# Kernel optimization log

Hardware: AMD Instinct MI355X
Metric: run time of the kernel (lower is better)

The kernel has to match this reference:

```python
import jax, jax.numpy as jnp
import numpy as np

HDIM = 256
VOCAB = 100000
NUM_CLASSES = 5
N_LEAVES = 2048


def _build_tree(n_leaves):
    # balanced pairing tree; leaves are nodes [0, n_leaves), internal nodes appended
    # in topological order so every parent index > its children's indices.
    frontier = list(range(n_leaves)); nid = n_leaves; left = []; right = []
    while len(frontier) > 1:
        nxt = []
        for a, b in zip(frontier[0::2], frontier[1::2]):
            left.append(a); right.append(b); nxt.append(nid); nid += 1
        if len(frontier) % 2 == 1:
            nxt.append(frontier[-1])
        frontier = nxt
    return np.asarray(left, np.int64), np.asarray(right, np.int64)


def setup_inputs() -> dict:
    key = jax.random.key(0)
    ks = jax.random.split(key, 12)
    left, right = _build_tree(N_LEAVES)
    s = 1.0 / float(np.sqrt(HDIM))
    W = lambda k, shp: (jax.random.normal(k, shp, jnp.float32) * s)
    z = lambda n: jnp.zeros((n,), jnp.float32)
    return {
        "word_ids": jax.random.randint(ks[0], (N_LEAVES,), 0, VOCAB),
        "left_idx": jnp.asarray(left),
        "right_idx": jnp.asarray(right),
        "emb": jax.random.normal(ks[1], (VOCAB, HDIM), jnp.float32) * 0.1,
        "Wi": W(ks[2], (HDIM, HDIM)), "bi": z(HDIM),
        "Wo": W(ks[3], (HDIM, HDIM)), "bo": z(HDIM),
        "Wu": W(ks[4], (HDIM, HDIM)), "bu": z(HDIM),
        "Ui": W(ks[5], (HDIM, 2 * HDIM)), "bui": z(HDIM),
        "Uo": W(ks[6], (HDIM, 2 * HDIM)), "buo": z(HDIM),
        "Uu": W(ks[7], (HDIM, 2 * HDIM)), "buu": z(HDIM),
        "Uf1": W(ks[8], (HDIM, HDIM)), "bf1": z(HDIM),
        "Uf2": W(ks[9], (HDIM, HDIM)), "bf2": z(HDIM),
        "Wp": W(ks[10], (NUM_CLASSES, HDIM)), "bp": z(NUM_CLASSES),
    }


def reference(word_ids, left_idx, right_idx, emb,
              Wi, bi, Wo, bo, Wu, bu,
              Ui, bui, Uo, buo, Uu, buu,
              Uf1, bf1, Uf2, bf2, Wp, bp):
    sig = jax.nn.sigmoid
    relu = jax.nn.relu
    n_leaves = word_ids.shape[0]
    n_internal = left_idx.shape[0]
    n_nodes = n_leaves + n_internal

    # --- leaf nodes, fully vectorized ---
    e = emb[word_ids]                                  # [L, H]
    i = sig(e @ Wi.T + bi)
    o = sig(e @ Wo.T + bo)
    u = relu(e @ Wu.T + bu)
    c_leaf = i * u
    h_leaf = o * relu(c_leaf)

    h_buf = jnp.zeros((n_nodes, HDIM), e.dtype).at[:n_leaves].set(h_leaf)
    node_ids = jnp.arange(n_leaves, n_nodes)

    # --- internal nodes: sequential by topological order ---
    def step(hb, xs):
        l, r, idx = xs
        lh = hb[l]; rh = hb[r]                         # [H] each
        cat = jnp.concatenate([lh, rh])                # [2H]
        ii = sig(Ui @ cat + bui)
        oo = sig(Uo @ cat + buo)
        uu = relu(Uu @ cat + buu)
        # NOTE: faithful to source — forget gates multiply child h, not child c
        c = ii * uu + sig(Uf1 @ lh + bf1) * lh + sig(Uf2 @ rh + bf2) * rh
        h = oo * relu(c)
        return hb.at[idx].set(h), None

    h_buf, _ = jax.lax.scan(step, h_buf, (left_idx, right_idx, node_ids))

    # per-node class logits (original concatenates projection(h) across all nodes)
    logits = h_buf @ Wp.T + bp                         # [n_nodes, numClasses]
    return logits
```

## Files before the change

kernel.cpp:

```cpp
#include <hip/hip_runtime.h>
#include <math.h>

#define H 256
#define KT 32
#define KTILES 16

__device__ __forceinline__ float sigmoidf_(float x) {
    return 1.0f / (1.0f + expf(-x));
}

__global__ __launch_bounds__(256) void pack_weights_kernel(
    const float* __restrict__ Wi, const float* __restrict__ Wo, const float* __restrict__ Wu,
    const float* __restrict__ Ui, const float* __restrict__ Uo, const float* __restrict__ Uu,
    const float* __restrict__ Uf1, const float* __restrict__ Uf2,
    float* __restrict__ dst)
{
    long idx = (long)blockIdx.x * 256 + threadIdx.x;
    const long W4N = 4L * 512 * 256;
    if (idx < W4N) {
        long g = idx >> 17;
        long r = idx & 131071;
        long k = r >> 8;
        long j = r & 255;
        float v;
        if      (g == 0) v = Ui[j * 512 + k];
        else if (g == 1) v = Uo[j * 512 + k];
        else if (g == 2) v = Uu[j * 512 + k];
        else             v = (k < 256) ? Uf1[j * 256 + k] : Uf2[j * 256 + (k - 256)];
        dst[idx] = v;
    } else {
        long t = idx - W4N;
        long g = t >> 16;
        long r = t & 65535;
        long k = r >> 8;
        long j = r & 255;
        const float* src = (g == 0) ? Wi : (g == 1) ? Wo : Wu;
        dst[idx] = src[j * 256 + k];
    }
}

template<int LPB>
__global__ __launch_bounds__(256) void leaf_kernel(
    const int* __restrict__ word_ids, const float* __restrict__ emb,
    const float* __restrict__ W3,
    const float* __restrict__ bi, const float* __restrict__ bo, const float* __restrict__ bu,
    float* __restrict__ h_buf)
{
    const int j = threadIdx.x;
    const int lbase = blockIdx.x * LPB;
    int wid[LPB];
#pragma unroll
    for (int l = 0; l < LPB; ++l)
        wid[l] = __builtin_amdgcn_readfirstlane(word_ids[lbase + l]);

    float ai[LPB], ao[LPB], au[LPB];
#pragma unroll
    for (int l = 0; l < LPB; ++l) { ai[l] = 0.f; ao[l] = 0.f; au[l] = 0.f; }

    const float* WiT = W3;
    const float* WoT = W3 + 65536;
    const float* WuT = W3 + 131072;

#pragma unroll 4
    for (int k = 0; k < H; ++k) {
        float wi = WiT[k * H + j];
        float wo = WoT[k * H + j];
        float wu = WuT[k * H + j];
#pragma unroll
        for (int l = 0; l < LPB; ++l) {
            float e = emb[(long)wid[l] * H + k];
            ai[l] = fmaf(e, wi, ai[l]);
            ao[l] = fmaf(e, wo, ao[l]);
            au[l] = fmaf(e, wu, au[l]);
        }
    }
    float bij = bi[j], boj = bo[j], buj = bu[j];
#pragma unroll
    for (int l = 0; l < LPB; ++l) {
        float ii = sigmoidf_(ai[l] + bij);
        float oo = sigmoidf_(ao[l] + boj);
        float uu = fmaxf(au[l] + buj, 0.f);
        float c  = ii * uu;
        float h  = oo * fmaxf(c, 0.f);
        h_buf[(long)(lbase + l) * H + j] = h;
    }
}

template<int NCH>
__global__ __launch_bounds__(256) void level_partial_kernel(
    const int* __restrict__ left_idx, const int* __restrict__ right_idx,
    const float* __restrict__ W4, const float* __restrict__ h_buf,
    float* __restrict__ part,
    int level_start, int chunk_base, int chunk_nodes, int n_leaves)
{
    const int j  = threadIdx.x;
    const int kt = blockIdx.x;
    const int nb = blockIdx.y * NCH;

    float w[4][KT];
#pragma unroll
    for (int g = 0; g < 4; ++g)
#pragma unroll
        for (int kk = 0; kk < KT; ++kk)
            w[g][kk] = W4[((long)g * 512 + kt * KT + kk) * H + j];

    const int  isLeft = (kt < 8);
    const int  k0 = (kt & 7) * KT;
    const int* cidx = isLeft ? left_idx : right_idx;

    const int nEnd = (nb + NCH < chunk_nodes) ? nb + NCH : chunk_nodes;
    for (int n = nb; n < nEnd; ++n) {
        int ti = level_start + chunk_base + n - n_leaves;
        int child = __builtin_amdgcn_readfirstlane(cidx[ti]);
        const float* row = h_buf + (long)child * H + k0;
        float a0 = 0.f, a1 = 0.f, a2 = 0.f, a3 = 0.f;
#pragma unroll
        for (int kk = 0; kk < KT; ++kk) {
            float x = row[kk];
            a0 = fmaf(x, w[0][kk], a0);
            a1 = fmaf(x, w[1][kk], a1);
            a2 = fmaf(x, w[2][kk], a2);
            a3 = fmaf(x, w[3][kk], a3);
        }
        float* p = part + (((long)n * KTILES + kt) * 4) * H + j;
        p[0]     = a0;
        p[H]     = a1;
        p[2 * H] = a2;
        p[3 * H] = a3;
    }
}

__global__ __launch_bounds__(256) void level_reduce_kernel(
    const int* __restrict__ left_idx, const int* __restrict__ right_idx,
    const float* __restrict__ part,
    const float* __restrict__ bui, const float* __restrict__ buo, const float* __restrict__ buu,
    const float* __restrict__ bf1, const float* __restrict__ bf2,
    float* __restrict__ h_buf,
    int level_start, int chunk_base, int n_leaves)
{
    const int j  = threadIdx.x;
    const int nc = blockIdx.x;

    float ai = 0.f, ao = 0.f, au = 0.f, af1 = 0.f, af2 = 0.f;
    const float* p = part + ((long)nc * KTILES * 4) * H + j;
#pragma unroll
    for (int kt = 0; kt < KTILES; ++kt) {
        const float* q = p + (long)kt * 4 * H;
        ai += q[0];
        ao += q[H];
        au += q[2 * H];
        if (kt < 8) af1 += q[3 * H]; else af2 += q[3 * H];
    }

    int node = level_start + chunk_base + nc;
    int ti   = node - n_leaves;
    int li   = left_idx[ti];
    int ri   = right_idx[ti];
    float lh = h_buf[(long)li * H + j];
    float rh = h_buf[(long)ri * H + j];

    float ii = sigmoidf_(ai  + bui[j]);
    float oo = sigmoidf_(ao  + buo[j]);
    float uu = fmaxf    (au  + buu[j], 0.f);
    float f1 = sigmoidf_(af1 + bf1[j]);
    float f2 = sigmoidf_(af2 + bf2[j]);
    float c  = ii * uu + f1 * lh + f2 * rh;
    float h  = oo * fmaxf(c, 0.f);
    h_buf[(long)node * H + j] = h;
}

__global__ __launch_bounds__(256) void proj_kernel(
    const float* __restrict__ h_buf, const float* __restrict__ Wp,
    const float* __restrict__ bp, float* __restrict__ out, int total)
{
    int t = blockIdx.x * 256 + threadIdx.x;
    if (t >= total) return;
    int node = t / 5;
    int cls  = t - node * 5;
    const float4* hr = (const float4*)(h_buf + (long)node * H);
    const float4* wr = (const float4*)(Wp + (long)cls * H);
    float acc = 0.f;
#pragma unroll 8
    for (int k = 0; k < H / 4; ++k) {
        float4 a = hr[k], b = wr[k];
        acc += a.x * b.x + a.y * b.y + a.z * b.z + a.w * b.w;
    }
    out[t] = acc + bp[cls];
}

extern "C" void kernel_launch(void* const* d_in, const int* in_sizes, int n_in,
                              void* d_out, int out_size, void* d_ws, size_t ws_size,
                              hipStream_t stream)
{
    const int*   word_ids  = (const int*)  d_in[0];
    const int*   left_idx  = (const int*)  d_in[1];
    const int*   right_idx = (const int*)  d_in[2];
    const float* emb       = (const float*)d_in[3];
    const float* Wi  = (const float*)d_in[4];  const float* bi  = (const float*)d_in[5];
    const float* Wo  = (const float*)d_in[6];  const float* bo  = (const float*)d_in[7];
    const float* Wu  = (const float*)d_in[8];  const float* bu  = (const float*)d_in[9];
    const float* Ui  = (const float*)d_in[10]; const float* bui = (const float*)d_in[11];
    const float* Uo  = (const float*)d_in[12]; const float* buo = (const float*)d_in[13];
    const float* Uu  = (const float*)d_in[14]; const float* buu = (const float*)d_in[15];
    const float* Uf1 = (const float*)d_in[16]; const float* bf1 = (const float*)d_in[17];
    const float* Uf2 = (const float*)d_in[18]; const float* bf2 = (const float*)d_in[19];
    const float* Wp  = (const float*)d_in[20]; const float* bp  = (const float*)d_in[21];

    const int n_leaves   = in_sizes[0];
    const int n_internal = in_sizes[1];
    const int n_nodes    = n_leaves + n_internal;

    float* ws    = (float*)d_ws;
    float* h_buf = ws;
    float* W4    = h_buf + (long)n_nodes * H;
    float* W3    = W4 + 4L * 512 * H;
    float* part  = W3 + 3L * 256 * H;
    (void)n_in; (void)out_size;

    long fixed_f = (long)n_nodes * H + 4L * 512 * H + 3L * 256 * H;
    long avail_f = (long)(ws_size / 4) - fixed_f;
    long per_node_f = (long)KTILES * 4 * H;
    int chunk_cap = (int)(avail_f / per_node_f);
    if (chunk_cap > 256) chunk_cap = 256;
    if (chunk_cap < 1)   chunk_cap = 1;

    pack_weights_kernel<<<2816, 256, 0, stream>>>(Wi, Wo, Wu, Ui, Uo, Uu, Uf1, Uf2, W4);

    constexpr int LPB = 8;
    leaf_kernel<LPB><<<n_leaves / LPB, 256, 0, stream>>>(
        word_ids, emb, W3, bi, bo, bu, h_buf);

    constexpr int NCH = 16;
    int frontier = n_leaves;
    int level_start = n_leaves;
    while (frontier > 1) {
        int cnt = frontier >> 1;
        for (int base = 0; base < cnt; base += chunk_cap) {
            int chunk = (cnt - base < chunk_cap) ? (cnt - base) : chunk_cap;
            dim3 gridA(KTILES, (chunk + NCH - 1) / NCH);
            level_partial_kernel<NCH><<<gridA, 256, 0, stream>>>(
                left_idx, right_idx, W4, h_buf, part,
                level_start, base, chunk, n_leaves);
            level_reduce_kernel<<<chunk, 256, 0, stream>>>(
                left_idx, right_idx, part,
                bui, buo, buu, bf1, bf2, h_buf,
                level_start, base, n_leaves);
        }
        level_start += cnt;
        frontier = cnt + (frontier & 1);
    }

    int total = n_nodes * 5;
    proj_kernel<<<(total + 255) / 256, 256, 0, stream>>>(h_buf, Wp, bp, (float*)d_out, total);
}
```

Baseline: 300.5 us.

## Replace multi-kernel level loop with single persistent cooperative tree kernel

Fuses weight packing, the leaf computation, all per-level partial/reduce launches and the final projection into one cooperative kernel that uses grid.sync between tree levels. Weights are read straight from the original layout into registers, and the K-tile partials are combined by an atomic last-arrival counter instead of a separate reduce launch. The projection is folded into each node's finalisation. This is meant to remove the many kernel launches per level, at the cost of grid-wide barriers, extra atomics and fences, larger workspace use, and host-side device property queries on every call.

```diff
diff --git a/kernel.cpp b/kernel.cpp
--- a/kernel.cpp
+++ b/kernel.cpp
@@ -1,255 +1,283 @@
 #include <hip/hip_runtime.h>
+#include <hip/hip_cooperative_groups.h>
 #include <math.h>
 
-#define H 256
+namespace cg = cooperative_groups;
+
+#define H  256
 #define KT 32
-#define KTILES 16
+
+struct Params {
+    const int *word_ids, *left_idx, *right_idx;
+    const float *emb;
+    const float *Wi, *bi, *Wo, *bo, *Wu, *bu;
+    const float *Ui, *bui, *Uo, *buo, *Uu, *buu;
+    const float *Uf1, *bf1, *Uf2, *bf2, *Wp, *bp;
+    float *h_buf;
+    float *part;
+    float *partL;
+    int   *cnt;
+    float *out;
+    int n_leaves, n_internal, n_nodes;
+};
 
 __device__ __forceinline__ float sigmoidf_(float x) {
     return 1.0f / (1.0f + expf(-x));
 }
 
-__global__ __launch_bounds__(256) void pack_weights_kernel(
-    const float* __restrict__ Wi, const float* __restrict__ Wo, const float* __restrict__ Wu,
-    const float* __restrict__ Ui, const float* __restrict__ Uo, const float* __restrict__ Uu,
-    const float* __restrict__ Uf1, const float* __restrict__ Uf2,
-    float* __restrict__ dst)
+__device__ __forceinline__ void proj_node(const Params& P, int node, float h,
+                                          int tid, float (*s_red)[5])
 {
-    long idx = (long)blockIdx.x * 256 + threadIdx.x;
-    const long W4N = 4L * 512 * 256;
-    if (idx < W4N) {
-        long g = idx >> 17;
-        long r = idx & 131071;
-        long k = r >> 8;
-        long j = r & 255;
-        float v;
-        if      (g == 0) v = Ui[j * 512 + k];
-        else if (g == 1) v = Uo[j * 512 + k];
-        else if (g == 2) v = Uu[j * 512 + k];
-        else             v = (k < 256) ? Uf1[j * 256 + k] : Uf2[j * 256 + (k - 256)];
-        dst[idx] = v;
-    } else {
-        long t = idx - W4N;
-        long g = t >> 16;
-        long r = t & 65535;
-        long k = r >> 8;
-        long j = r & 255;
-        const float* src = (g == 0) ? Wi : (g == 1) ? Wo : Wu;
-        dst[idx] = src[j * 256 + k];
-    }
-}
-
-template<int LPB>
-__global__ __launch_bounds__(256) void leaf_kernel(
-    const int* __restrict__ word_ids, const float* __restrict__ emb,
-    const float* __restrict__ W3,
-    const float* __restrict__ bi, const float* __restrict__ bo, const float* __restrict__ bu,
-    float* __restrict__ h_buf)
+    const int j = tid;
+    float p0 = P.Wp[0 * H + j] * h;
+    float p1 = P.Wp[1 * H + j] * h;
+    float p2 = P.Wp[2 * H + j] * h;
+    float p3 = P.Wp[3 * H + j] * h;
+    float p4 = P.Wp[4 * H + j] * h;
+#pragma unroll
+    for (int off = 32; off >= 1; off >>= 1) {
+        p0 += __shfl_down(p0, off);
+        p1 += __shfl_down(p1, off);
+        p2 += __shfl_down(p2, off);
+        p3 += __shfl_down(p3, off);
+        p4 += __shfl_down(p4, off);
+    }
+    int lane = tid & 63, wv = tid >> 6;
+    if (lane == 0) {
+        s_red[wv][0] = p0; s_red[wv][1] = p1; s_red[wv][2] = p2;
+        s_red[wv][3] = p3; s_red[wv][4] = p4;
+    }
+    __syncthreads();
+    if (tid < 5)
+        P.out[(size_t)node * 5 + tid] =
+            P.bp[tid] + s_red[0][tid] + s_red[1][tid] + s_red[2][tid] + s_red[3][tid];
+    __syncthreads();
+}
+
+__global__ __launch_bounds__(256, 2) void tree_kernel(Params P)
 {
-    const int j = threadIdx.x;
-    const int lbase = blockIdx.x * LPB;
-    int wid[LPB];
-#pragma unroll
-    for (int l = 0; l < LPB; ++l)
-        wid[l] = __builtin_amdgcn_readfirstlane(word_ids[lbase + l]);
-
-    float ai[LPB], ao[LPB], au[LPB];
-#pragma unroll
-    for (int l = 0; l < LPB; ++l) { ai[l] = 0.f; ao[l] = 0.f; au[l] = 0.f; }
-
-    const float* WiT = W3;
-    const float* WoT = W3 + 65536;
-    const float* WuT = W3 + 131072;
-
-#pragma unroll 4
-    for (int k = 0; k < H; ++k) {
-        float wi = WiT[k * H + j];
-        float wo = WoT[k * H + j];
-        float wu = WuT[k * H + j];
-#pragma unroll
-        for (int l = 0; l < LPB; ++l) {
-            float e = emb[(long)wid[l] * H + k];
-            ai[l] = fmaf(e, wi, ai[l]);
-            ao[l] = fmaf(e, wo, ao[l]);
-            au[l] = fmaf(e, wu, au[l]);
-        }
-    }
-    float bij = bi[j], boj = bo[j], buj = bu[j];
-#pragma unroll
-    for (int l = 0; l < LPB; ++l) {
-        float ii = sigmoidf_(ai[l] + bij);
-        float oo = sigmoidf_(ao[l] + boj);
-        float uu = fmaxf(au[l] + buj, 0.f);
-        float c  = ii * uu;
-        float h  = oo * fmaxf(c, 0.f);
-        h_buf[(long)(lbase + l) * H + j] = h;
-    }
-}
-
-template<int NCH>
-__global__ __launch_bounds__(256) void level_partial_kernel(
-    const int* __restrict__ left_idx, const int* __restrict__ right_idx,
-    const float* __restrict__ W4, const float* __restrict__ h_buf,
-    float* __restrict__ part,
-    int level_start, int chunk_base, int chunk_nodes, int n_leaves)
-{
-    const int j  = threadIdx.x;
-    const int kt = blockIdx.x;
-    const int nb = blockIdx.y * NCH;
-
-    float w[4][KT];
-#pragma unroll
-    for (int g = 0; g < 4; ++g)
-#pragma unroll
-        for (int kk = 0; kk < KT; ++kk)
-            w[g][kk] = W4[((long)g * 512 + kt * KT + kk) * H + j];
-
-    const int  isLeft = (kt < 8);
-    const int  k0 = (kt & 7) * KT;
-    const int* cidx = isLeft ? left_idx : right_idx;
-
-    const int nEnd = (nb + NCH < chunk_nodes) ? nb + NCH : chunk_nodes;
-    for (int n = nb; n < nEnd; ++n) {
-        int ti = level_start + chunk_base + n - n_leaves;
-        int child = __builtin_amdgcn_readfirstlane(cidx[ti]);
-        const float* row = h_buf + (long)child * H + k0;
-        float a0 = 0.f, a1 = 0.f, a2 = 0.f, a3 = 0.f;
-#pragma unroll
-        for (int kk = 0; kk < KT; ++kk) {
-            float x = row[kk];
-            a0 = fmaf(x, w[0][kk], a0);
-            a1 = fmaf(x, w[1][kk], a1);
-            a2 = fmaf(x, w[2][kk], a2);
-            a3 = fmaf(x, w[3][kk], a3);
-        }
-        float* p = part + (((long)n * KTILES + kt) * 4) * H + j;
-        p[0]     = a0;
-        p[H]     = a1;
-        p[2 * H] = a2;
-        p[3 * H] = a3;
-    }
-}
-
-__global__ __launch_bounds__(256) void level_reduce_kernel(
-    const int* __restrict__ left_idx, const int* __restrict__ right_idx,
-    const float* __restrict__ part,
-    const float* __restrict__ bui, const float* __restrict__ buo, const float* __restrict__ buu,
-    const float* __restrict__ bf1, const float* __restrict__ bf2,
-    float* __restrict__ h_buf,
-    int level_start, int chunk_base, int n_leaves)
-{
-    const int j  = threadIdx.x;
-    const int nc = blockIdx.x;
-
-    float ai = 0.f, ao = 0.f, au = 0.f, af1 = 0.f, af2 = 0.f;
-    const float* p = part + ((long)nc * KTILES * 4) * H + j;
-#pragma unroll
-    for (int kt = 0; kt < KTILES; ++kt) {
-        const float* q = p + (long)kt * 4 * H;
-        ai += q[0];
-        ao += q[H];
-        au += q[2 * H];
-        if (kt < 8) af1 += q[3 * H]; else af2 += q[3 * H];
-    }
-
-    int node = level_start + chunk_base + nc;
-    int ti   = node - n_leaves;
-    int li   = left_idx[ti];
-    int ri   = right_idx[ti];
-    float lh = h_buf[(long)li * H + j];
-    float rh = h_buf[(long)ri * H + j];
-
-    float ii = sigmoidf_(ai  + bui[j]);
-    float oo = sigmoidf_(ao  + buo[j]);
-    float uu = fmaxf    (au  + buu[j], 0.f);
-    float f1 = sigmoidf_(af1 + bf1[j]);
-    float f2 = sigmoidf_(af2 + bf2[j]);
-    float c  = ii * uu + f1 * lh + f2 * rh;
-    float h  = oo * fmaxf(c, 0.f);
-    h_buf[(long)node * H + j] = h;
-}
-
-__global__ __launch_bounds__(256) void proj_kernel(
-    const float* __restrict__ h_buf, const float* __restrict__ Wp,
-    const float* __restrict__ bp, float* __restrict__ out, int total)
-{
-    int t = blockIdx.x * 256 + threadIdx.x;
-    if (t >= total) return;
-    int node = t / 5;
-    int cls  = t - node * 5;
-    const float4* hr = (const float4*)(h_buf + (long)node * H);
-    const float4* wr = (const float4*)(Wp + (long)cls * H);
-    float acc = 0.f;
-#pragma unroll 8
-    for (int k = 0; k < H / 4; ++k) {
-        float4 a = hr[k], b = wr[k];
-        acc += a.x * b.x + a.y * b.y + a.z * b.z + a.w * b.w;
-    }
-    out[t] = acc + bp[cls];
+    cg::grid_group grid = cg::this_grid();
+    const int tid = threadIdx.x;
+    const int b   = blockIdx.x;
+    const int G   = gridDim.x;
+    const int j   = tid;
+
+    __shared__ int   s_win[128];
+    __shared__ float s_red[4][5];
+
+    for (int i = b * 256 + tid; i < P.n_nodes; i += G * 256) P.cnt[i] = 0;
+    grid.sync();
+
+    float wA[KT], wB[KT], wC[KT], wD[KT];
+
+    {
+        const int NLC = G >> 3;
+        const int ktl = b & 7;
+        const int lco = b >> 3;
+        const int k0  = ktl * KT;
+        const float4* q0 = (const float4*)(P.Wi + (size_t)j * H + k0);
+        const float4* q1 = (const float4*)(P.Wo + (size_t)j * H + k0);
+        const float4* q2 = (const float4*)(P.Wu + (size_t)j * H + k0);
+#pragma unroll
+        for (int q = 0; q < KT / 4; ++q) {
+            float4 v0 = q0[q], v1 = q1[q], v2 = q2[q];
+            wA[4*q] = v0.x; wA[4*q+1] = v0.y; wA[4*q+2] = v0.z; wA[4*q+3] = v0.w;
+            wB[4*q] = v1.x; wB[4*q+1] = v1.y; wB[4*q+2] = v1.z; wB[4*q+3] = v1.w;
+            wC[4*q] = v2.x; wC[4*q+1] = v2.y; wC[4*q+2] = v2.z; wC[4*q+3] = v2.w;
+        }
+        for (int base = lco; base < P.n_leaves; base += NLC * 128) {
+            int nit = 0;
+            for (int it = 0; it < 128; ++it) {
+                int l = base + it * NLC;
+                if (l >= P.n_leaves) break;
+                ++nit;
+                int wid = __builtin_amdgcn_readfirstlane(P.word_ids[l]);
+                const float* row = P.emb + (size_t)wid * H + k0;
+                float a0 = 0.f, a1 = 0.f, a2 = 0.f;
+#pragma unroll
+                for (int kk = 0; kk < KT; ++kk) {
+                    float x = row[kk];
+                    a0 = fmaf(x, wA[kk], a0);
+                    a1 = fmaf(x, wB[kk], a1);
+                    a2 = fmaf(x, wC[kk], a2);
+                }
+                float* p = P.partL + (((size_t)l * 8 + ktl) * 3) * H + j;
+                p[0]     = a0;
+                p[H]     = a1;
+                p[2 * H] = a2;
+            }
+            __threadfence();
+            __syncthreads();
+            if (tid < nit) {
+                int l = base + tid * NLC;
+                int old = atomicAdd(&P.cnt[l], 1);
+                s_win[tid] = (old == 7) ? 1 : 0;
+            }
+            __syncthreads();
+            bool fenced = false;
+            for (int it = 0; it < nit; ++it) {
+                if (!s_win[it]) continue;
+                if (!fenced) { __threadfence(); fenced = true; }
+                int l = base + it * NLC;
+                const float* p = P.partL + ((size_t)l * 8 * 3) * H + j;
+                float ai = P.bi[j], ao = P.bo[j], au = P.bu[j];
+#pragma unroll
+                for (int k2 = 0; k2 < 8; ++k2) {
+                    const float* q = p + (size_t)k2 * 3 * H;
+                    ai += q[0];
+                    ao += q[H];
+                    au += q[2 * H];
+                }
+                float ii = sigmoidf_(ai);
+                float oo = sigmoidf_(ao);
+                float uu = fmaxf(au, 0.f);
+                float c  = ii * uu;
+                float h  = oo * fmaxf(c, 0.f);
+                P.h_buf[(size_t)l * H + j] = h;
+                proj_node(P, l, h, tid, s_red);
+            }
+            __syncthreads();
+        }
+    }
+    grid.sync();
+
+    {
+        const int kt  = b & 15;
+        const int coh = b >> 4;
+        const int NC  = G >> 4;
+        const int k0  = (kt & 7) * KT;
+        const float4* q0 = (const float4*)(P.Ui + (size_t)j * 2 * H + kt * KT);
+        const float4* q1 = (const float4*)(P.Uo + (size_t)j * 2 * H + kt * KT);
+        const float4* q2 = (const float4*)(P.Uu + (size_t)j * 2 * H + kt * KT);
+        const float*  fsrc = (kt < 8) ? P.Uf1 : P.Uf2;
+        const float4* q3 = (const float4*)(fsrc + (size_t)j * H + k0);
+#pragma unroll
+        for (int q = 0; q < KT / 4; ++q) {
+            float4 v0 = q0[q], v1 = q1[q], v2 = q2[q], v3 = q3[q];
+            wA[4*q] = v0.x; wA[4*q+1] = v0.y; wA[4*q+2] = v0.z; wA[4*q+3] = v0.w;
+            wB[4*q] = v1.x; wB[4*q+1] = v1.y; wB[4*q+2] = v1.z; wB[4*q+3] = v1.w;
+            wC[4*q] = v2.x; wC[4*q+1] = v2.y; wC[4*q+2] = v2.z; wC[4*q+3] = v2.w;
+            wD[4*q] = v3.x; wD[4*q+1] = v3.y; wD[4*q+2] = v3.z; wD[4*q+3] = v3.w;
+        }
+        const int* cidx = (kt < 8) ? P.left_idx : P.right_idx;
+
+        int frontier = P.n_leaves;
+        int tbase = 0;
+        while (frontier > 1) {
+            int lvl = frontier >> 1;
+            for (int base = 0; base < lvl; base += NC * 128) {
+                int nit = 0;
+                for (int it = 0; it < 128; ++it) {
+                    int t = tbase + base + coh + it * NC;
+                    if (base + coh + it * NC >= lvl) break;
+                    ++nit;
+                    int child = __builtin_amdgcn_readfirstlane(cidx[t]);
+                    const float* row = P.h_buf + (size_t)child * H + k0;
+                    float a0 = 0.f, a1 = 0.f, a2 = 0.f, a3 = 0.f;
+#pragma unroll
+                    for (int kk = 0; kk < KT; ++kk) {
+                        float x = row[kk];
+                        a0 = fmaf(x, wA[kk], a0);
+                        a1 = fmaf(x, wB[kk], a1);
+                        a2 = fmaf(x, wC[kk], a2);
+                        a3 = fmaf(x, wD[kk], a3);
+                    }
+                    float* p = P.part + (((size_t)t * 16 + kt) * 4) * H + j;
+                    p[0]     = a0;
+                    p[H]     = a1;
+                    p[2 * H] = a2;
+                    p[3 * H] = a3;
+                }
+                __threadfence();
+                __syncthreads();
+                if (tid < nit) {
+                    int t = tbase + base + coh + tid * NC;
+                    int old = atomicAdd(&P.cnt[P.n_leaves + t], 1);
+                    s_win[tid] = (old == 15) ? 1 : 0;
+                }
+                __syncthreads();
+                bool fenced = false;
+                for (int it = 0; it < nit; ++it) {
+                    if (!s_win[it]) continue;
+                    if (!fenced) { __threadfence(); fenced = true; }
+                    int t = tbase + base + coh + it * NC;
+                    const float* p = P.part + ((size_t)t * 16 * 4) * H + j;
+                    float ai = P.bui[j], ao = P.buo[j], au = P.buu[j];
+                    float f1 = P.bf1[j], f2 = P.bf2[j];
+#pragma unroll
+                    for (int k2 = 0; k2 < 16; ++k2) {
+                        const float* q = p + (size_t)k2 * 4 * H;
+                        ai += q[0];
+                        ao += q[H];
+                        au += q[2 * H];
+                        float fv = q[3 * H];
+                        if (k2 < 8) f1 += fv; else f2 += fv;
+                    }
+                    int li = P.left_idx[t], ri = P.right_idx[t];
+                    float lh = P.h_buf[(size_t)li * H + j];
+                    float rh = P.h_buf[(size_t)ri * H + j];
+                    float ii  = sigmoidf_(ai);
+                    float oo  = sigmoidf_(ao);
+                    float uu  = fmaxf(au, 0.f);
+                    float ff1 = sigmoidf_(f1);
+                    float ff2 = sigmoidf_(f2);
+                    float c   = ii * uu + ff1 * lh + ff2 * rh;
+                    float h   = oo * fmaxf(c, 0.f);
+                    int node  = P.n_leaves + t;
+                    P.h_buf[(size_t)node * H + j] = h;
+                    proj_node(P, node, h, tid, s_red);
+                }
+                __syncthreads();
+            }
+            grid.sync();
+            tbase += lvl;
+            frontier = lvl + (frontier & 1);
+        }
+    }
 }
 
 extern "C" void kernel_launch(void* const* d_in, const int* in_sizes, int n_in,
                               void* d_out, int out_size, void* d_ws, size_t ws_size,
                               hipStream_t stream)
 {
-    const int*   word_ids  = (const int*)  d_in[0];
-    const int*   left_idx  = (const int*)  d_in[1];
-    const int*   right_idx = (const int*)  d_in[2];
-    const float* emb       = (const float*)d_in[3];
-    const float* Wi  = (const float*)d_in[4];  const float* bi  = (const float*)d_in[5];
-    const float* Wo  = (const float*)d_in[6];  const float* bo  = (const float*)d_in[7];
-    const float* Wu  = (const float*)d_in[8];  const float* bu  = (const float*)d_in[9];
-    const float* Ui  = (const float*)d_in[10]; const float* bui = (const float*)d_in[11];
-    const float* Uo  = (const float*)d_in[12]; const float* buo = (const float*)d_in[13];
-    const float* Uu  = (const float*)d_in[14]; const float* buu = (const float*)d_in[15];
-    const float* Uf1 = (const float*)d_in[16]; const float* bf1 = (const float*)d_in[17];
-    const float* Uf2 = (const float*)d_in[18]; const float* bf2 = (const float*)d_in[19];
-    const float* Wp  = (const float*)d_in[20]; const float* bp  = (const float*)d_in[21];
-
-    const int n_leaves   = in_sizes[0];
-    const int n_internal = in_sizes[1];
-    const int n_nodes    = n_leaves + n_internal;
-
-    float* ws    = (float*)d_ws;
-    float* h_buf = ws;
-    float* W4    = h_buf + (long)n_nodes * H;
-    float* W3    = W4 + 4L * 512 * H;
-    float* part  = W3 + 3L * 256 * H;
-    (void)n_in; (void)out_size;
-
-    long fixed_f = (long)n_nodes * H + 4L * 512 * H + 3L * 256 * H;
-    long avail_f = (long)(ws_size / 4) - fixed_f;
-    long per_node_f = (long)KTILES * 4 * H;
-    int chunk_cap = (int)(avail_f / per_node_f);
-    if (chunk_cap > 256) chunk_cap = 256;
-    if (chunk_cap < 1)   chunk_cap = 1;
-
-    pack_weights_kernel<<<2816, 256, 0, stream>>>(Wi, Wo, Wu, Ui, Uo, Uu, Uf1, Uf2, W4);
-
-    constexpr int LPB = 8;
-    leaf_kernel<LPB><<<n_leaves / LPB, 256, 0, stream>>>(
-        word_ids, emb, W3, bi, bo, bu, h_buf);
-
-    constexpr int NCH = 16;
-    int frontier = n_leaves;
-    int level_start = n_leaves;
-    while (frontier > 1) {
-        int cnt = frontier >> 1;
-        for (int base = 0; base < cnt; base += chunk_cap) {
-            int chunk = (cnt - base < chunk_cap) ? (cnt - base) : chunk_cap;
-            dim3 gridA(KTILES, (chunk + NCH - 1) / NCH);
-            level_partial_kernel<NCH><<<gridA, 256, 0, stream>>>(
-                left_idx, right_idx, W4, h_buf, part,
-                level_start, base, chunk, n_leaves);
-            level_reduce_kernel<<<chunk, 256, 0, stream>>>(
-                left_idx, right_idx, part,
-                bui, buo, buu, bf1, bf2, h_buf,
-                level_start, base, n_leaves);
-        }
-        level_start += cnt;
-        frontier = cnt + (frontier & 1);
-    }
-
-    int total = n_nodes * 5;
-    proj_kernel<<<(total + 255) / 256, 256, 0, stream>>>(h_buf, Wp, bp, (float*)d_out, total);
-}
+    Params P;
+    P.word_ids  = (const int*)d_in[0];
+    P.left_idx  = (const int*)d_in[1];
+    P.right_idx = (const int*)d_in[2];
+    P.emb = (const float*)d_in[3];
+    P.Wi  = (const float*)d_in[4];  P.bi  = (const float*)d_in[5];
+    P.Wo  = (const float*)d_in[6];  P.bo  = (const float*)d_in[7];
+    P.Wu  = (const float*)d_in[8];  P.bu  = (const float*)d_in[9];
+    P.Ui  = (const float*)d_in[10]; P.bui = (const float*)d_in[11];
+    P.Uo  = (const float*)d_in[12]; P.buo = (const float*)d_in[13];
+    P.Uu  = (const float*)d_in[14]; P.buu = (const float*)d_in[15];
+    P.Uf1 = (const float*)d_in[16]; P.bf1 = (const float*)d_in[17];
+    P.Uf2 = (const float*)d_in[18]; P.bf2 = (const float*)d_in[19];
+    P.Wp  = (const float*)d_in[20]; P.bp  = (const float*)d_in[21];
+    P.n_leaves   = in_sizes[0];
+    P.n_internal = in_sizes[1];
+    P.n_nodes    = P.n_leaves + P.n_internal;
+    P.out = (float*)d_out;
+    (void)n_in; (void)out_size; (void)ws_size;
+
+    float* ws = (float*)d_ws;
+    P.h_buf = ws;
+    P.part  = P.h_buf + (size_t)P.n_nodes * H;
+    P.partL = P.part  + (size_t)P.n_internal * 16 * 4 * H;
+    P.cnt   = (int*)(P.partL + (size_t)P.n_leaves * 8 * 3 * H);
+
+    int dev = 0;
+    hipGetDevice(&dev);
+    hipDeviceProp_t props;
+    hipGetDeviceProperties(&props, dev);
+    int perCU = 0;
+    hipOccupancyMaxActiveBlocksPerMultiprocessor(&perCU, (const void*)tree_kernel, 256, 0);
+    if (perCU < 1) perCU = 1;
+    long Gl = (long)perCU * props.multiProcessorCount;
+    int G = (Gl > 512) ? 512 : (int)Gl;
+    G &= ~15;
+    if (G < 16) G = 16;
+
+    void* args[] = { &P };
+    hipLaunchCooperativeKernel((void*)tree_kernel, dim3(G), dim3(256), args, 0, stream);
+}
```

Result: slower. 1.131 ms (+276.4%).
